# Kernel optimization log

Measured on AMD Instinct MI355X. Metric: run time of the kernel, lower is better.

Reference implementation:

```python
import jax, jax.numpy as jnp
import numpy as np

B, D, C = 8192, 1024, 8  # batch, input_size, n_conditions


def setup_inputs() -> dict:
    key = jax.random.key(0)
    k1, k2, k3, k4 = jax.random.split(key, 4)
    x = jax.random.normal(k1, (B, D), dtype=jnp.float32)
    condition_ids = jax.random.randint(k2, (B,), 0, C)  # metadata[batch_key] codes
    # Per-condition Linear(D, D) weights (torch layout: [out, in]) and biases
    W = jax.random.normal(k3, (C, D, D), dtype=jnp.float32) / np.sqrt(D)
    b = jax.random.normal(k4, (C, D), dtype=jnp.float32) * 0.01
    return {"x": x, "condition_ids": condition_ids, "W": W, "b": b}


def reference(x, condition_ids, W, b):
    # Original: for each condition c, zero non-member rows of x, apply
    # Linear_c to the FULL batch, then sum partials. Because Linear is
    # affine, the summed result per row is:
    #   out[i] = W[c_i] @ x[i] + sum_c b_c
    # (each bias b_c is added to EVERY row since the Linear runs on the
    #  full masked batch). We keep the dense per-condition GEMM structure.
    onehot = jax.nn.one_hot(condition_ids, C, dtype=x.dtype)  # [B, C]
    y = jnp.einsum('bi,coi->cbo', x, W)                       # [C, B, D]
    out = jnp.einsum('cbo,bc->bo', y, onehot) + b.sum(axis=0)  # [B, D]
    return out
```

## Files before the change

kernel.cpp:

```cpp
#include <hip/hip_runtime.h>
#include <hip/hip_bf16.h>
#include <cstdint>

#define B_ROWS 8192
#define DIM    1024
#define NC     8
#define NXCD   8
#define SLOTS  16
#define BM     128
#define BN     64
#define NT     16

typedef __bf16 bf16;
typedef __bf16 bf16x4 __attribute__((ext_vector_type(4)));
typedef __bf16 bf16x8 __attribute__((ext_vector_type(8)));
typedef float  f32x4  __attribute__((ext_vector_type(4)));

typedef __attribute__((address_space(3))) void* lds_vp;
typedef const __attribute__((address_space(1))) void* gbl_vp;

#define BUFB 24576
#define ABYT 16384

#define XF4 (B_ROWS * DIM / 4)
__global__ __launch_bounds__(1024) void prep_kernel(
    const float* __restrict__ x, const float* __restrict__ W,
    const int* __restrict__ ids, const float* __restrict__ b,
    bf16* __restrict__ xb, bf16* __restrict__ wb,
    int* __restrict__ row_list, int* __restrict__ xmeta,
    float* __restrict__ bias_sum) {
    if (blockIdx.x != 0) {
        size_t base = (size_t)(blockIdx.x - 1) * 8192 + threadIdx.x;
        const float4* src;
        bf16* dst;
        if (base < (size_t)XF4) { src = (const float4*)x; dst = xb; }
        else                    { src = (const float4*)W; dst = wb; base -= (size_t)XF4; }
        float4 v[8];
#pragma unroll
        for (int k = 0; k < 8; k++) v[k] = src[base + (size_t)k * 1024];
#pragma unroll
        for (int k = 0; k < 8; k++) {
            bf16x4 o;
            o[0] = (bf16)v[k].x; o[1] = (bf16)v[k].y;
            o[2] = (bf16)v[k].z; o[3] = (bf16)v[k].w;
            *(bf16x4*)(dst + 4 * (base + (size_t)k * 1024)) = o;
        }
        return;
    }
    __shared__ int wtot_s[16][NC];
    __shared__ int cnt_s[NC];
    __shared__ int off_s[NC];
    __shared__ int used_s[NXCD];
    __shared__ int novf_s[NC];
    int tid = threadIdx.x, lane = tid & 63, wv = tid >> 6;
    const int per = B_ROWS / 1024;
    int base = tid * per;

    if (tid < NXCD * SLOTS) xmeta[tid * 3 + 2] = 0;

    const int4* idv = (const int4*)(ids + base);
    int4 v0 = idv[0], v1 = idv[1];
    int myid[8] = {v0.x, v0.y, v0.z, v0.w, v1.x, v1.y, v1.z, v1.w};
    unsigned long long p0 = 0, p1 = 0;
#pragma unroll
    for (int q = 0; q < 8; q++) {
        int id = myid[q];
        unsigned long long one = 1ull << ((id & 3) << 4);
        if (id < 4) p0 += one; else p1 += one;
    }
    unsigned long long i0 = p0, i1 = p1;
#pragma unroll
    for (int d = 1; d < 64; d <<= 1) {
        unsigned long long u0 = __shfl_up(i0, d, 64);
        unsigned long long u1 = __shfl_up(i1, d, 64);
        if (lane >= d) { i0 += u0; i1 += u1; }
    }
    unsigned long long e0 = i0 - p0, e1 = i1 - p1;
    unsigned long long t0 = __shfl(i0, 63, 64), t1 = __shfl(i1, 63, 64);
    if (lane == 0) {
#pragma unroll
        for (int c = 0; c < 4; c++) {
            wtot_s[wv][c]     = (int)((t0 >> (c << 4)) & 0xFFFF);
            wtot_s[wv][c + 4] = (int)((t1 >> (c << 4)) & 0xFFFF);
        }
    }
    __syncthreads();
    if (tid < NC) {
        int acc = 0;
        for (int w2 = 0; w2 < 16; w2++) { int t = wtot_s[w2][tid]; wtot_s[w2][tid] = acc; acc += t; }
        cnt_s[tid] = acc;
    }
    __syncthreads();
    if (tid < NC) {
        int acc = 0;
        for (int c2 = 0; c2 < tid; c2++) acc += cnt_s[c2];
        off_s[tid] = acc;
    }
    __syncthreads();
    if (tid < 16 * NC) wtot_s[tid >> 3][tid & 7] += off_s[tid & 7];
    __syncthreads();

    if (tid < NC) {
        int c = tid, n = cnt_s[c];
        int tc = (n + BM - 1) >> 7;
        int prim = tc < SLOTS ? tc : SLOTS;
        for (int t = 0; t < prim; t++) {
            int* e = xmeta + (c * SLOTS + t) * 3;
            int rc = n - t * BM; if (rc > BM) rc = BM;
            e[0] = c; e[1] = off_s[c] + t * BM; e[2] = rc;
        }
        used_s[c] = prim;
        novf_s[c] = tc - prim;
    }
    {
        float s = 0.f;
#pragma unroll
        for (int c = 0; c < NC; c++) s += b[c * DIM + tid];
        bias_sum[tid] = s;
    }
    __syncthreads();
    if (tid == 0) {
        int k = 0;
        for (int c = 0; c < NC; c++) {
            for (int t = 0; t < novf_s[c]; t++) {
                for (;;) {
                    int xx = k >> 4, s = k & (SLOTS - 1); k++;
                    if (s >= used_s[xx]) {
                        int* e = xmeta + (xx * SLOTS + s) * 3;
                        int rc = cnt_s[c] - (SLOTS + t) * BM; if (rc > BM) rc = BM;
                        e[0] = c; e[1] = off_s[c] + (SLOTS + t) * BM; e[2] = rc;
                        break;
                    }
                }
            }
        }
    }
    unsigned long long r0 = 0, r1 = 0;
#pragma unroll
    for (int j = 0; j < per; j++) {
        int id = myid[j];
        int sh = (id & 3) << 4;
        unsigned long long run = (id < 4) ? r0 : r1;
        unsigned long long exc = (id < 4) ? e0 : e1;
        int p = wtot_s[wv][id] + (int)((exc >> sh) & 0xFFFF) + (int)((run >> sh) & 0xFFFF);
        row_list[p] = base + j;
        unsigned long long one = 1ull << sh;
        if (id < 4) r0 += one; else r1 += one;
    }
}

__global__ __launch_bounds__(256, 3) void gemm_kernel(
    const bf16* __restrict__ xb, const bf16* __restrict__ wb,
    const float* __restrict__ bias_sum, const int* __restrict__ row_list,
    const int* __restrict__ xmeta, float* __restrict__ out) {
    int xcd = blockIdx.x, slot = blockIdx.y, colt = blockIdx.z;
    const int* e = xmeta + (xcd * SLOTS + slot) * 3;
    int cond = e[0], rstart = e[1], rcnt = e[2];
    if (rcnt == 0) return;
    int col0 = colt * BN;

    __shared__ char lds[2 * BUFB];

    int tid  = threadIdx.x;
    int lane = tid & 63;
    int w    = tid >> 6;
    int wr   = w >> 1;
    int wc   = w & 1;
    int srow = lane >> 3;
    int scol = ((lane & 7) ^ srow) * 8;

    const bf16 *aS[4], *bS[2];
#pragma unroll
    for (int i = 0; i < 4; i++) {
        int tr = i * 32 + w * 8 + srow;
        int rr = (tr < rcnt) ? tr : 0;
        int grow = row_list[rstart + rr];
        aS[i] = xb + (size_t)grow * DIM + scol;
    }
#pragma unroll
    for (int i = 0; i < 2; i++) {
        int br = i * 32 + w * 8 + srow;
        bS[i] = wb + (size_t)cond * DIM * DIM + (size_t)(col0 + br) * DIM + scol;
    }

    f32x4 acc[4][2];
#pragma unroll
    for (int m = 0; m < 4; m++)
#pragma unroll
        for (int n = 0; n < 2; n++) acc[m][n] = (f32x4){0.f, 0.f, 0.f, 0.f};

    int fr = lane & 15;
    int fq = lane >> 4;
    int off0 = (fq * 16) ^ ((fr & 7) << 4);
    int off1 = off0 ^ 64;

    auto stage = [&](int buf, int k0) {
#pragma unroll
        for (int i = 0; i < 4; i++)
            __builtin_amdgcn_global_load_lds((gbl_vp)(aS[i] + k0),
                (lds_vp)(lds + buf * BUFB + (i * 32 + w * 8) * 128), 16, 0, 0);
#pragma unroll
        for (int i = 0; i < 2; i++)
            __builtin_amdgcn_global_load_lds((gbl_vp)(bS[i] + k0),
                (lds_vp)(lds + buf * BUFB + ABYT + (i * 32 + w * 8) * 128), 16, 0, 0);
    };

    stage(0, 0);
    stage(1, 64);

    for (int t = 0; t < NT; ++t) {
        if (t < NT - 1) asm volatile("s_waitcnt vmcnt(6)" ::: "memory");
        else            asm volatile("s_waitcnt vmcnt(0)" ::: "memory");
        __builtin_amdgcn_s_barrier();

        const char* bA = lds + (t & 1) * BUFB + (wr * 64 + fr) * 128;
        const char* bB = lds + (t & 1) * BUFB + ABYT + (wc * 32 + fr) * 128;
#pragma unroll
        for (int kk = 0; kk < 2; ++kk) {
            int ofs = kk ? off1 : off0;
            bf16x8 af[4], bv[2];
#pragma unroll
            for (int m = 0; m < 4; m++) af[m] = *(const bf16x8*)(bA + m * 2048 + ofs);
#pragma unroll
            for (int n = 0; n < 2; n++) bv[n] = *(const bf16x8*)(bB + n * 2048 + ofs);
            __builtin_amdgcn_s_setprio(1);
#pragma unroll
            for (int m = 0; m < 4; m++)
#pragma unroll
                for (int n = 0; n < 2; n++)
                    acc[m][n] = __builtin_amdgcn_mfma_f32_16x16x32_bf16(
                        af[m], bv[n], acc[m][n], 0, 0, 0);
            __builtin_amdgcn_s_setprio(0);
        }

        asm volatile("s_waitcnt lgkmcnt(0)" ::: "memory");
        __builtin_amdgcn_s_barrier();
        if (t + 2 < NT) stage(t & 1, (t + 2) * 64);
    }

    float bias[2];
#pragma unroll
    for (int n = 0; n < 2; n++) bias[n] = bias_sum[col0 + wc * 32 + n * 16 + fr];
#pragma unroll
    for (int m = 0; m < 4; m++) {
#pragma unroll
        for (int i = 0; i < 4; i++) {
            int rl = wr * 64 + m * 16 + fq * 4 + i;
            if (rl < rcnt) {
                int grow = row_list[rstart + rl];
                float* op = out + (size_t)grow * DIM + col0 + wc * 32 + fr;
#pragma unroll
                for (int n = 0; n < 2; n++) op[n * 16] = acc[m][n][i] + bias[n];
            }
        }
    }
}

__global__ void naive_kernel(const float* __restrict__ x, const int* __restrict__ ids,
                             const float* __restrict__ W, const float* __restrict__ b,
                             float* __restrict__ out) {
    int row = blockIdx.x;
    int c = ids[row];
    __shared__ float xs[DIM];
    for (int i = threadIdx.x; i < DIM; i += 256) xs[i] = x[(size_t)row * DIM + i];
    __syncthreads();
    const float* Wc = W + (size_t)c * DIM * DIM;
    for (int o = threadIdx.x; o < DIM; o += 256) {
        float s = 0.f;
        const float* wrp = Wc + (size_t)o * DIM;
        for (int i = 0; i < DIM; i++) s += xs[i] * wrp[i];
        float bs = 0.f;
#pragma unroll
        for (int cc = 0; cc < NC; cc++) bs += b[cc * DIM + o];
        out[(size_t)row * DIM + o] = s + bs;
    }
}

extern "C" void kernel_launch(void* const* d_in, const int* in_sizes, int n_in,
                              void* d_out, int out_size, void* d_ws, size_t ws_size,
                              hipStream_t stream) {
    const float* x   = (const float*)d_in[0];
    const int*   ids = (const int*)d_in[1];
    const float* W   = (const float*)d_in[2];
    const float* b   = (const float*)d_in[3];
    float*       out = (float*)d_out;

    size_t xb_off   = 0;
    size_t xb_sz    = (size_t)B_ROWS * DIM * 2;
    size_t wb_off   = (xb_off + xb_sz + 255) & ~(size_t)255;
    size_t wb_sz    = (size_t)NC * DIM * DIM * 2;
    size_t bias_off = (wb_off + wb_sz + 255) & ~(size_t)255;
    size_t rl_off   = (bias_off + DIM * 4 + 255) & ~(size_t)255;
    size_t meta_off = (rl_off + B_ROWS * 4 + 255) & ~(size_t)255;
    size_t need     = meta_off + (size_t)NXCD * SLOTS * 3 * 4;

    if (ws_size < need) {
        naive_kernel<<<dim3(B_ROWS), dim3(256), 0, stream>>>(x, ids, W, b, out);
        return;
    }

    char* ws = (char*)d_ws;
    bf16*  xb       = (bf16*)(ws + xb_off);
    bf16*  wbf      = (bf16*)(ws + wb_off);
    float* bias_sum = (float*)(ws + bias_off);
    int*   row_list = (int*)(ws + rl_off);
    int*   xmeta    = (int*)(ws + meta_off);

    prep_kernel<<<dim3(513), dim3(1024), 0, stream>>>(x, W, ids, b, xb, wbf,
                                                      row_list, xmeta, bias_sum);
    gemm_kernel<<<dim3(NXCD, SLOTS, DIM / BN), dim3(256), 0, stream>>>(
        xb, wbf, bias_sum, row_list, xmeta, out);
}
```

Before: 52.68 us.

## Fuse weight fp32-to-bf16 conversion into GEMM B-tile staging

The prep kernel no longer converts W to bf16 in a workspace; the GEMM now loads fp32 W rows into registers, converts them to bf16 and writes them into swizzled LDS, pipelined one stage ahead. This removes a full read and write pass over the 32MB weight tensor and halves the prep grid. In exchange, each W tile is read as fp32 (twice the bytes) by every row-slot block that shares it, and the B staging goes through registers with extra waitcnt bookkeeping instead of direct global-to-LDS loads.

```diff
diff --git a/kernel.cpp b/kernel.cpp
--- a/kernel.cpp
+++ b/kernel.cpp
@@ -24,17 +24,13 @@
 
 #define XF4 (B_ROWS * DIM / 4)
 __global__ __launch_bounds__(1024) void prep_kernel(
-    const float* __restrict__ x, const float* __restrict__ W,
-    const int* __restrict__ ids, const float* __restrict__ b,
-    bf16* __restrict__ xb, bf16* __restrict__ wb,
+    const float* __restrict__ x, const int* __restrict__ ids,
+    const float* __restrict__ b, bf16* __restrict__ xb,
     int* __restrict__ row_list, int* __restrict__ xmeta,
     float* __restrict__ bias_sum) {
     if (blockIdx.x != 0) {
         size_t base = (size_t)(blockIdx.x - 1) * 8192 + threadIdx.x;
-        const float4* src;
-        bf16* dst;
-        if (base < (size_t)XF4) { src = (const float4*)x; dst = xb; }
-        else                    { src = (const float4*)W; dst = wb; base -= (size_t)XF4; }
+        const float4* src = (const float4*)x;
         float4 v[8];
 #pragma unroll
         for (int k = 0; k < 8; k++) v[k] = src[base + (size_t)k * 1024];
@@ -43,7 +39,7 @@
             bf16x4 o;
             o[0] = (bf16)v[k].x; o[1] = (bf16)v[k].y;
             o[2] = (bf16)v[k].z; o[3] = (bf16)v[k].w;
-            *(bf16x4*)(dst + 4 * (base + (size_t)k * 1024)) = o;
+            *(bf16x4*)(xb + 4 * (base + (size_t)k * 1024)) = o;
         }
         return;
     }
@@ -150,7 +146,7 @@
 }
 
 __global__ __launch_bounds__(256, 3) void gemm_kernel(
-    const bf16* __restrict__ xb, const bf16* __restrict__ wb,
+    const bf16* __restrict__ xb, const float* __restrict__ W,
     const float* __restrict__ bias_sum, const int* __restrict__ row_list,
     const int* __restrict__ xmeta, float* __restrict__ out) {
     int xcd = blockIdx.x, slot = blockIdx.y, colt = blockIdx.z;
@@ -169,7 +165,7 @@
     int srow = lane >> 3;
     int scol = ((lane & 7) ^ srow) * 8;
 
-    const bf16 *aS[4], *bS[2];
+    const bf16* aS[4];
 #pragma unroll
     for (int i = 0; i < 4; i++) {
         int tr = i * 32 + w * 8 + srow;
@@ -177,11 +173,12 @@
         int grow = row_list[rstart + rr];
         aS[i] = xb + (size_t)grow * DIM + scol;
     }
-#pragma unroll
-    for (int i = 0; i < 2; i++) {
-        int br = i * 32 + w * 8 + srow;
-        bS[i] = wb + (size_t)cond * DIM * DIM + (size_t)(col0 + br) * DIM + scol;
-    }
+    int brow = tid >> 2;
+    int kseg = tid & 3;
+    const float* bW = W + (size_t)cond * DIM * DIM + (size_t)(col0 + brow) * DIM + kseg * 16;
+    int g0 = kseg * 2;
+    int bofs0 = ABYT + brow * 128 + ((g0 * 16) ^ ((brow & 7) << 4));
+    int bofs1 = ABYT + brow * 128 + (((g0 + 1) * 16) ^ ((brow & 7) << 4));
 
     f32x4 acc[4][2];
 #pragma unroll
@@ -194,22 +191,39 @@
     int off0 = (fq * 16) ^ ((fr & 7) << 4);
     int off1 = off0 ^ 64;
 
-    auto stage = [&](int buf, int k0) {
+    float4 vb[4];
+
+    auto LOADB = [&](int k0) {
+        const float4* p = (const float4*)(bW + k0);
+#pragma unroll
+        for (int j = 0; j < 4; j++) vb[j] = p[j];
+    };
+    auto WRITEB = [&](int buf) {
+        bf16x8 o0, o1;
+        o0[0] = (bf16)vb[0].x; o0[1] = (bf16)vb[0].y; o0[2] = (bf16)vb[0].z; o0[3] = (bf16)vb[0].w;
+        o0[4] = (bf16)vb[1].x; o0[5] = (bf16)vb[1].y; o0[6] = (bf16)vb[1].z; o0[7] = (bf16)vb[1].w;
+        o1[0] = (bf16)vb[2].x; o1[1] = (bf16)vb[2].y; o1[2] = (bf16)vb[2].z; o1[3] = (bf16)vb[2].w;
+        o1[4] = (bf16)vb[3].x; o1[5] = (bf16)vb[3].y; o1[6] = (bf16)vb[3].z; o1[7] = (bf16)vb[3].w;
+        *(bf16x8*)(lds + buf * BUFB + bofs0) = o0;
+        *(bf16x8*)(lds + buf * BUFB + bofs1) = o1;
+    };
+    auto STAGEA = [&](int buf, int k0) {
 #pragma unroll
         for (int i = 0; i < 4; i++)
             __builtin_amdgcn_global_load_lds((gbl_vp)(aS[i] + k0),
                 (lds_vp)(lds + buf * BUFB + (i * 32 + w * 8) * 128), 16, 0, 0);
-#pragma unroll
-        for (int i = 0; i < 2; i++)
-            __builtin_amdgcn_global_load_lds((gbl_vp)(bS[i] + k0),
-                (lds_vp)(lds + buf * BUFB + ABYT + (i * 32 + w * 8) * 128), 16, 0, 0);
     };
 
-    stage(0, 0);
-    stage(1, 64);
+    LOADB(0);
+    STAGEA(0, 0);
+    asm volatile("s_waitcnt vmcnt(4)" ::: "memory");
+    WRITEB(0);
+    LOADB(64);
+    STAGEA(1, 64);
+    asm volatile("s_waitcnt lgkmcnt(0)" ::: "memory");
 
     for (int t = 0; t < NT; ++t) {
-        if (t < NT - 1) asm volatile("s_waitcnt vmcnt(6)" ::: "memory");
+        if (t < NT - 1) asm volatile("s_waitcnt vmcnt(8)" ::: "memory");
         else            asm volatile("s_waitcnt vmcnt(0)" ::: "memory");
         __builtin_amdgcn_s_barrier();
 
@@ -233,9 +247,16 @@
             __builtin_amdgcn_s_setprio(0);
         }
 
+        if (t + 1 < NT) {
+            asm volatile("s_waitcnt vmcnt(4)" ::: "memory");
+            WRITEB((t + 1) & 1);
+        }
         asm volatile("s_waitcnt lgkmcnt(0)" ::: "memory");
         __builtin_amdgcn_s_barrier();
-        if (t + 2 < NT) stage(t & 1, (t + 2) * 64);
+        if (t + 2 < NT) {
+            LOADB((t + 2) * 64);
+            STAGEA(t & 1, (t + 2) * 64);
+        }
     }
 
     float bias[2];
@@ -287,9 +308,7 @@
 
     size_t xb_off   = 0;
     size_t xb_sz    = (size_t)B_ROWS * DIM * 2;
-    size_t wb_off   = (xb_off + xb_sz + 255) & ~(size_t)255;
-    size_t wb_sz    = (size_t)NC * DIM * DIM * 2;
-    size_t bias_off = (wb_off + wb_sz + 255) & ~(size_t)255;
+    size_t bias_off = (xb_off + xb_sz + 255) & ~(size_t)255;
     size_t rl_off   = (bias_off + DIM * 4 + 255) & ~(size_t)255;
     size_t meta_off = (rl_off + B_ROWS * 4 + 255) & ~(size_t)255;
     size_t need     = meta_off + (size_t)NXCD * SLOTS * 3 * 4;
@@ -301,13 +320,12 @@
 
     char* ws = (char*)d_ws;
     bf16*  xb       = (bf16*)(ws + xb_off);
-    bf16*  wbf      = (bf16*)(ws + wb_off);
     float* bias_sum = (float*)(ws + bias_off);
     int*   row_list = (int*)(ws + rl_off);
     int*   xmeta    = (int*)(ws + meta_off);
 
-    prep_kernel<<<dim3(513), dim3(1024), 0, stream>>>(x, W, ids, b, xb, wbf,
+    prep_kernel<<<dim3(257), dim3(1024), 0, stream>>>(x, ids, b, xb,
                                                       row_list, xmeta, bias_sum);
     gemm_kernel<<<dim3(NXCD, SLOTS, DIM / BN), dim3(256), 0, stream>>>(
-        xb, wbf, bias_sum, row_list, xmeta, out);
+        xb, W, bias_sum, row_list, xmeta, out);
 }
```

Result: slower. 62.66 us (+18.9%).
